# Kernel tuning notes

Hardware: AMD Instinct MI355X
Metric: run time of the kernel (lower is better)

Reference implementation:

```python
import jax, jax.numpy as jnp
import numpy as np

N = 100000  # nodes
E = 1600000  # edges


def gcn_conv(x, W, b, src, dst, n_nodes):
    """PyG-style GCNConv: add self-loops, symmetric norm, linear, scatter-add, bias."""
    h = x @ W  # [N, F_out]
    loop = jnp.arange(n_nodes, dtype=src.dtype)
    s = jnp.concatenate([src, loop])  # source nodes (messages flow src -> dst)
    d = jnp.concatenate([dst, loop])
    deg = jax.ops.segment_sum(jnp.ones_like(d, dtype=h.dtype), d, num_segments=n_nodes)
    dinv = jnp.where(deg > 0, jax.lax.rsqrt(deg), 0.0)
    norm = dinv[s] * dinv[d]  # [E+N]
    msgs = h[s] * norm[:, None]  # [E+N, F_out] -- dominant memory traffic
    out = jax.ops.segment_sum(msgs, d, num_segments=n_nodes)
    return out + b


def setup_inputs() -> dict:
    key = jax.random.key(0)
    k1, k2, k3, k4 = jax.random.split(key, 4)
    x = jax.random.normal(k1, (N, 128), dtype=jnp.float32)
    edge_index = jax.random.randint(k2, (2, E), 0, N, dtype=jnp.int32)
    W1 = jax.random.normal(k3, (128, 64), dtype=jnp.float32) * (1.0 / np.sqrt(128))
    b1 = jnp.zeros((64,), dtype=jnp.float32)
    W2 = jax.random.normal(k4, (64, 16), dtype=jnp.float32) * (1.0 / np.sqrt(64))
    b2 = jnp.zeros((16,), dtype=jnp.float32)
    return {"x": x, "edge_index": edge_index, "W1": W1, "b1": b1, "W2": W2, "b2": b2}


def reference(x, edge_index, W1, b1, W2, b2):
    src, dst = edge_index[0], edge_index[1]
    h = gcn_conv(x, W1, b1, src, dst, N)
    h = jax.nn.leaky_relu(h, negative_slope=0.2)
    # dropout is identity in eval mode
    h = gcn_conv(h, W2, b2, src, dst, N)
    return jax.nn.log_softmax(h, axis=-1)
```

## Files before the change

### kernel.cpp

```cpp
#include <hip/hip_runtime.h>
#include <math.h>


#define CHUNK 4096
#define BSHIFT 9
#define BMASK 511
#define CAP 9216

typedef __bf16 bf16x8 __attribute__((ext_vector_type(8)));
typedef float f32x4 __attribute__((ext_vector_type(4)));

__device__ __forceinline__ unsigned f2b(float f) {
  unsigned u = __float_as_uint(f);
  return (u + 0x7FFF + ((u >> 16) & 1)) >> 16;
}

__global__ void binit_kernel(int* __restrict__ gbcursor, int nbc,
                             unsigned* __restrict__ h1s, int n) {
  int b = blockIdx.x * 256 + threadIdx.x;
  if (b < nbc) gbcursor[b] = b * CAP;
  if (blockIdx.x == 0 && threadIdx.x < 32) h1s[(size_t)n * 32 + threadIdx.x] = 0u;
}

__global__ __launch_bounds__(256) void scatterA_kernel(const int* __restrict__ src,
                                                       const int* __restrict__ dst,
                                                       int E, int nbc,
                                                       int* __restrict__ gbcursor,
                                                       int* __restrict__ tmp) {
  __shared__ int hist[256];
  __shared__ int segcur[256];
  int tid = threadIdx.x;
  int estart = blockIdx.x * CHUNK;
  int eend = min(E, estart + CHUNK);
  hist[tid] = 0;
  __syncthreads();
  for (int i = estart + tid; i < eend; i += 256)
    atomicAdd(&hist[dst[i] >> BSHIFT], 1);
  __syncthreads();
  if (tid < nbc) {
    int c = hist[tid];
    segcur[tid] = c ? atomicAdd(&gbcursor[tid], c) : 0;
  }
  __syncthreads();
  for (int i = estart + tid; i < eend; i += 256) {
    int d = dst[i];
    int b = d >> BSHIFT;
    int pos = atomicAdd(&segcur[b], 1);
    if (pos < (b + 1) * CAP)
      tmp[pos] = (src[i] << BSHIFT) | (d & BMASK);
  }
}

__global__ __launch_bounds__(1024) void csrbuild_kernel(const int* __restrict__ tmp,
                                                        const int* __restrict__ gbcursor,
                                                        int n, int* __restrict__ row_start,
                                                        int* __restrict__ degs,
                                                        float* __restrict__ dinv,
                                                        int* __restrict__ csr) {
  __shared__ int nh[512];
  __shared__ int sc[512];
  __shared__ int lcur[512];
  int b = blockIdx.x, tid = threadIdx.x;
  int base = b * CAP;
  int count = min(gbcursor[b] - base, CAP);
  if (tid < 512) nh[tid] = 0;
  __syncthreads();
  for (int i = tid; i < count; i += 1024) atomicAdd(&nh[tmp[base + i] & BMASK], 1);
  __syncthreads();
  int d = 0;
  if (tid < 512) { d = nh[tid]; sc[tid] = d; }
  __syncthreads();
  for (int off = 1; off < 512; off <<= 1) {
    int a = 0;
    if (tid < 512) { a = sc[tid]; if (tid >= off) a += sc[tid - off]; }
    __syncthreads();
    if (tid < 512) sc[tid] = a;
    __syncthreads();
  }
  if (tid < 512) {
    int e0 = base + sc[tid] - d;
    lcur[tid] = e0;
    int v = (b << BSHIFT) + tid;
    if (v < n) {
      row_start[v] = e0; degs[v] = d;
      dinv[v] = rsqrtf((float)(d + 1));
    }
  }
  __syncthreads();
  for (int i = tid; i < count; i += 1024) {
    int val = tmp[base + i];
    int pos = atomicAdd(&lcur[val & BMASK], 1);
    csr[pos] = val >> BSHIFT;
  }
}

__global__ __launch_bounds__(256, 4) void gemm1_kernel(const float* __restrict__ x,
                                                       const float* __restrict__ W1,
                                                       const float* __restrict__ dinv,
                                                       unsigned* __restrict__ h1s, int n) {
  __shared__ unsigned lds_u[64 * 68 * 2];
  unsigned* xs = lds_u;
  unsigned* wt = lds_u + 64 * 68;
  int tid = threadIdx.x;
  int vb = blockIdx.x * 64;
  int nrows = min(64, n - vb);

  const float4* xg = (const float4*)(x + (size_t)vb * 128);
#pragma unroll
  for (int it = 0; it < 8; ++it) {
    int idx = it * 256 + tid;
    int r = idx >> 5, c2 = idx & 31;
    float4 vv = make_float4(0.f, 0.f, 0.f, 0.f);
    if (r < nrows) vv = xg[idx];
    xs[r * 68 + c2 * 2] = (f2b(vv.y) << 16) | f2b(vv.x);
    xs[r * 68 + c2 * 2 + 1] = (f2b(vv.w) << 16) | f2b(vv.z);
  }
  unsigned short* wt16 = (unsigned short*)wt;
  const float4* wg = (const float4*)W1;
#pragma unroll
  for (int it = 0; it < 8; ++it) {
    int idx = it * 256 + tid;
    int k = idx >> 4, n0 = (idx & 15) * 4;
    float4 wv = wg[idx];
    wt16[(n0 + 0) * 136 + k] = (unsigned short)f2b(wv.x);
    wt16[(n0 + 1) * 136 + k] = (unsigned short)f2b(wv.y);
    wt16[(n0 + 2) * 136 + k] = (unsigned short)f2b(wv.z);
    wt16[(n0 + 3) * 136 + k] = (unsigned short)f2b(wv.w);
  }
  __syncthreads();

  int lane = tid & 63, wid = tid >> 6;
  int m16 = lane & 15, quad = lane >> 4;
  const unsigned* xp = xs + (wid * 16 + m16) * 68 + quad * 4;
  const unsigned* wp = wt + m16 * 68 + quad * 4;
  f32x4 acc[4] = {};
#pragma unroll
  for (int ks = 0; ks < 4; ++ks) {
    bf16x8 a = *(const bf16x8*)(xp + ks * 16);
#pragma unroll
    for (int nt = 0; nt < 4; ++nt) {
      bf16x8 b = *(const bf16x8*)(wp + nt * 16 * 68 + ks * 16);
      acc[nt] = __builtin_amdgcn_mfma_f32_16x16x32_bf16(a, b, acc[nt], 0, 0, 0);
    }
  }
  int rbase = vb + wid * 16 + quad * 4;
  float dvv[4];
#pragma unroll
  for (int reg = 0; reg < 4; ++reg) {
    int row = rbase + reg;
    dvv[reg] = (row < n) ? dinv[row] : 0.f;
  }
  unsigned short* h16 = (unsigned short*)h1s;
#pragma unroll
  for (int nt = 0; nt < 4; ++nt) {
    int col = nt * 16 + m16;
#pragma unroll
    for (int reg = 0; reg < 4; ++reg) {
      int row = rbase + reg;
      if (row < n)
        h16[(size_t)row * 64 + col] = (unsigned short)f2b(dvv[reg] * acc[nt][reg]);
    }
  }
}

struct f2 { float x, y; };
__device__ __forceinline__ void addu(f2& a, unsigned u) {
  a.x += __uint_as_float(u << 16);
  a.y += __uint_as_float(u);
}
__device__ __forceinline__ void addu4(f2* a, uint4 g) {
  addu(a[0], g.x); addu(a[1], g.y); addu(a[2], g.z); addu(a[3], g.w);
}

__global__ __launch_bounds__(256) void agg1_kernel(const uint4* __restrict__ h1s4,
                                                   const float* __restrict__ dinv,
                                                   const int* __restrict__ row_start,
                                                   const int* __restrict__ degs,
                                                   const int* __restrict__ csr,
                                                   const float* __restrict__ b1,
                                                   const float* __restrict__ W2,
                                                   unsigned* __restrict__ t, int n) {
  __shared__ float W2s[64 * 17];
  __shared__ float b1s[64];
  __shared__ float a_s[4][2][64];
  for (int i = threadIdx.x; i < 1024; i += 256)
    W2s[(i >> 4) * 17 + (i & 15)] = W2[i];
  if (threadIdx.x < 64) b1s[threadIdx.x] = b1[threadIdx.x];
  if (blockIdx.x == 0 && threadIdx.x < 8) t[(size_t)n * 8 + threadIdx.x] = 0u;
  __syncthreads();

  int wave = threadIdx.x >> 6, lane = threadIdx.x & 63;
  int half = lane >> 5, sub = lane & 31;
  int e = sub >> 3, c = sub & 7;
  int j = sub & 15, grp = (sub >> 4) & 1;

  for (int vbase = blockIdx.x * 8; vbase < n; vbase += gridDim.x * 8) {
    int v = vbase + wave * 2 + half;
    bool valid = (v < n);
    int vc = valid ? v : 0;
    int i = row_start[vc];
    int e1 = i + (valid ? degs[vc] : 0);
    float dv = valid ? dinv[vc] : 0.f;

    f2 a0[4];
#pragma unroll
    for (int k = 0; k < 4; ++k) a0[k] = {0.f, 0.f};
    {
      int s = (valid && sub < 8) ? v : n;
      addu4(a0, h1s4[(size_t)s * 8 + c]);
    }
    while (__any(i < e1)) {
      int i0 = i + e, i1 = i + 4 + e;
      int s0v = csr[i0];
      int s1v = csr[i1];
      int s0 = (i0 < e1) ? s0v : n;
      int s1 = (i1 < e1) ? s1v : n;
      uint4 g0 = h1s4[(size_t)s0 * 8 + c];
      uint4 g1 = h1s4[(size_t)s1 * 8 + c];
      addu4(a0, g0);
      addu4(a0, g1);
      i += 8;
    }
#pragma unroll
    for (int m = 8; m <= 16; m <<= 1) {
#pragma unroll
      for (int k = 0; k < 4; ++k) {
        a0[k].x += __shfl_xor(a0[k].x, m, 64);
        a0[k].y += __shfl_xor(a0[k].y, m, 64);
      }
    }
    if (sub < 8) {
#pragma unroll
      for (int k = 0; k < 4; ++k) {
        float z0 = fmaf(dv, a0[k].x, b1s[8 * sub + 2 * k]);
        float z1 = fmaf(dv, a0[k].y, b1s[8 * sub + 2 * k + 1]);
        a_s[wave][half][8 * sub + 2 * k] = fmaxf(z0, 0.2f * z0);
        a_s[wave][half][8 * sub + 2 * k + 1] = fmaxf(z1, 0.2f * z1);
      }
    }
    float p = 0.f;
#pragma unroll
    for (int q = 0; q < 16; ++q) {
      int f = grp * 16 + q;
      p = fmaf(a_s[wave][half][f], W2s[f * 17 + j], p);
    }
#pragma unroll
    for (int q = 0; q < 16; ++q) {
      int f = 32 + grp * 16 + q;
      p = fmaf(a_s[wave][half][f], W2s[f * 17 + j], p);
    }
    p += __shfl_xor(p, 16, 64);
    float pv = dv * p;
    float po = __shfl_xor(pv, 1, 64);
    if (valid && sub < 16 && !(sub & 1))
      t[(size_t)v * 8 + (sub >> 1)] = (f2b(po) << 16) | f2b(pv);
  }
}

__global__ __launch_bounds__(256) void agg2_kernel(const uint4* __restrict__ t4,
                                                   const float* __restrict__ dinv,
                                                   const int* __restrict__ row_start,
                                                   const int* __restrict__ degs,
                                                   const int* __restrict__ csr,
                                                   const float* __restrict__ b2,
                                                   float* __restrict__ out, int n) {
  int idx = blockIdx.x * 256 + threadIdx.x;
  int v = idx >> 4;
  if (v >= n) return;
  int sub = threadIdx.x & 15;
  int e = sub >> 1, c = sub & 1;
  float dv = dinv[v];
  int e0 = row_start[v], e1 = e0 + degs[v];
  f2 A0[4], A1[4];
#pragma unroll
  for (int k = 0; k < 4; ++k) { A0[k] = {0.f, 0.f}; A1[k] = {0.f, 0.f}; }
  {
    int s = (e == 0) ? v : n;
    addu4(A0, t4[(size_t)s * 2 + c]);
  }
  int i = e0;
  while (i + 8 < e1) {
    int i1 = i + 8 + e;
    int s0 = csr[i + e];
    int s1v = csr[i1];
    int s1 = (i1 < e1) ? s1v : n;
    uint4 g0 = t4[(size_t)s0 * 2 + c];
    uint4 g1 = t4[(size_t)s1 * 2 + c];
    addu4(A0, g0);
    addu4(A1, g1);
    i += 16;
  }
  if (i < e1) {
    int i0 = i + e;
    int sv = csr[i0];
    int s = (i0 < e1) ? sv : n;
    addu4(A0, t4[(size_t)s * 2 + c]);
  }
#pragma unroll
  for (int k = 0; k < 4; ++k) { A0[k].x += A1[k].x; A0[k].y += A1[k].y; }
#pragma unroll
  for (int m = 2; m <= 8; m <<= 1) {
#pragma unroll
    for (int k = 0; k < 4; ++k) {
      A0[k].x += __shfl_xor(A0[k].x, m, 64);
      A0[k].y += __shfl_xor(A0[k].y, m, 64);
    }
  }
  float4 bb0 = ((const float4*)b2)[c * 2];
  float4 bb1 = ((const float4*)b2)[c * 2 + 1];
  float z[8];
  z[0] = fmaf(dv, A0[0].x, bb0.x); z[1] = fmaf(dv, A0[0].y, bb0.y);
  z[2] = fmaf(dv, A0[1].x, bb0.z); z[3] = fmaf(dv, A0[1].y, bb0.w);
  z[4] = fmaf(dv, A0[2].x, bb1.x); z[5] = fmaf(dv, A0[2].y, bb1.y);
  z[6] = fmaf(dv, A0[3].x, bb1.z); z[7] = fmaf(dv, A0[3].y, bb1.w);
  float mx = z[0];
#pragma unroll
  for (int q = 1; q < 8; ++q) mx = fmaxf(mx, z[q]);
  mx = fmaxf(mx, __shfl_xor(mx, 1, 64));
  float ss = 0.f;
#pragma unroll
  for (int q = 0; q < 8; ++q) ss += expf(z[q] - mx);
  ss += __shfl_xor(ss, 1, 64);
  float lg = mx + logf(ss);
  if (e == 0) {
    float4 r0 = make_float4(z[0] - lg, z[1] - lg, z[2] - lg, z[3] - lg);
    float4 r1 = make_float4(z[4] - lg, z[5] - lg, z[6] - lg, z[7] - lg);
    float4* o = (float4*)out + (size_t)v * 4 + c * 2;
    o[0] = r0;
    o[1] = r1;
  }
}

extern "C" void kernel_launch(void* const* d_in, const int* in_sizes, int n_in,
                              void* d_out, int out_size, void* d_ws, size_t ws_size,
                              hipStream_t stream) {
  const float* x = (const float*)d_in[0];
  const int* edge_index = (const int*)d_in[1];
  const float* W1 = (const float*)d_in[2];
  const float* b1 = (const float*)d_in[3];
  const float* W2 = (const float*)d_in[4];
  const float* b2 = (const float*)d_in[5];
  float* out = (float*)d_out;

  int N_ = in_sizes[0] / 128;
  int E_ = in_sizes[1] / 2;
  const int* src = edge_index;
  const int* dst = edge_index + E_;
  int NBc = (N_ + BMASK) >> BSHIFT;

  char* ws = (char*)d_ws;
  size_t off = 0;
  auto take = [&](size_t bytes) {
    void* p = ws + off;
    off += (bytes + 255) & ~(size_t)255;
    return p;
  };
  unsigned* h1s = (unsigned*)take(((size_t)N_ + 1) * 32 * 4);
  size_t t_bytes = ((size_t)N_ + 1) * 8 * 4, tmp_bytes = (size_t)NBc * CAP * 4;
  void* t_union = take(t_bytes > tmp_bytes ? t_bytes : tmp_bytes);
  unsigned* t = (unsigned*)t_union;
  int* tmp = (int*)t_union;
  float* dinv = (float*)take((size_t)N_ * 4);
  int* degs = (int*)take((size_t)N_ * 4);
  int* row_start = (int*)take(((size_t)N_ + 1) * 4);
  int* csr = (int*)take(((size_t)NBc * CAP + 16) * 4);
  int* gbcursor = (int*)take((size_t)NBc * 4);
  (void)ws_size;

  binit_kernel<<<(NBc + 255) / 256, 256, 0, stream>>>(gbcursor, NBc, h1s, N_);
  scatterA_kernel<<<(E_ + CHUNK - 1) / CHUNK, 256, 0, stream>>>(src, dst, E_, NBc,
                                                                gbcursor, tmp);
  csrbuild_kernel<<<NBc, 1024, 0, stream>>>(tmp, gbcursor, N_, row_start, degs,
                                            dinv, csr);
  gemm1_kernel<<<(N_ + 63) / 64, 256, 0, stream>>>(x, W1, dinv, h1s, N_);
  agg1_kernel<<<2048, 256, 0, stream>>>((const uint4*)h1s, dinv, row_start, degs,
                                        csr, b1, W2, t, N_);
  agg2_kernel<<<(N_ * 16 + 255) / 256, 256, 0, stream>>>((const uint4*)t, dinv,
                                                         row_start, degs, csr,
                                                         b2, out, N_);
}
```

Measured before the change: 212.2 us.

## Fuse CSR build into layer-1 aggregation using LDS-resident bucket adjacency

Splits the CSR build into a lightweight degree-count kernel, which feeds dinv to the GEMM, and moves the bucket sort into the layer-1 aggregation kernel. Each 1024-thread block now sorts its 512-node bucket into shared memory and aggregates directly from that local CSR, writing the global CSR only for layer 2. It also prefetches the first 32 neighbor indices and gathers into registers to raise memory-level parallelism in both aggregation kernels. The costs are one extra pass over tmp and a grid of only about 196 large blocks with heavy LDS use, which may reduce occupancy. tmp and t no longer share a buffer.

```diff
diff --git a/kernel.cpp b/kernel.cpp
--- a/kernel.cpp
+++ b/kernel.cpp
@@ -6,6 +6,7 @@
 #define BSHIFT 9
 #define BMASK 511
 #define CAP 9216
+#define CAPP (CAP + 40)
 
 typedef __bf16 bf16x8 __attribute__((ext_vector_type(8)));
 typedef float f32x4 __attribute__((ext_vector_type(4)));
@@ -15,11 +16,24 @@
   return (u + 0x7FFF + ((u >> 16) & 1)) >> 16;
 }
 
+struct f2 { float x, y; };
+__device__ __forceinline__ void addu(f2& a, unsigned u) {
+  a.x += __uint_as_float(u << 16);
+  a.y += __uint_as_float(u & 0xffff0000u);
+}
+__device__ __forceinline__ void addu4(f2* a, uint4 g) {
+  addu(a[0], g.x); addu(a[1], g.y); addu(a[2], g.z); addu(a[3], g.w);
+}
+
 __global__ void binit_kernel(int* __restrict__ gbcursor, int nbc,
-                             unsigned* __restrict__ h1s, int n) {
+                             unsigned* __restrict__ h1s, unsigned* __restrict__ t,
+                             int n) {
   int b = blockIdx.x * 256 + threadIdx.x;
   if (b < nbc) gbcursor[b] = b * CAP;
-  if (blockIdx.x == 0 && threadIdx.x < 32) h1s[(size_t)n * 32 + threadIdx.x] = 0u;
+  if (blockIdx.x == 0) {
+    if (threadIdx.x < 32) h1s[(size_t)n * 32 + threadIdx.x] = 0u;
+    else if (threadIdx.x < 40) t[(size_t)n * 8 + (threadIdx.x - 32)] = 0u;
+  }
 }
 
 __global__ __launch_bounds__(256) void scatterA_kernel(const int* __restrict__ src,
@@ -51,47 +65,19 @@
   }
 }
 
-__global__ __launch_bounds__(1024) void csrbuild_kernel(const int* __restrict__ tmp,
-                                                        const int* __restrict__ gbcursor,
-                                                        int n, int* __restrict__ row_start,
-                                                        int* __restrict__ degs,
-                                                        float* __restrict__ dinv,
-                                                        int* __restrict__ csr) {
+__global__ __launch_bounds__(512) void degcnt_kernel(const int* __restrict__ tmp,
+                                                     const int* __restrict__ gbcursor,
+                                                     float* __restrict__ dinv, int n) {
   __shared__ int nh[512];
-  __shared__ int sc[512];
-  __shared__ int lcur[512];
   int b = blockIdx.x, tid = threadIdx.x;
+  nh[tid] = 0;
+  __syncthreads();
   int base = b * CAP;
   int count = min(gbcursor[b] - base, CAP);
-  if (tid < 512) nh[tid] = 0;
-  __syncthreads();
-  for (int i = tid; i < count; i += 1024) atomicAdd(&nh[tmp[base + i] & BMASK], 1);
-  __syncthreads();
-  int d = 0;
-  if (tid < 512) { d = nh[tid]; sc[tid] = d; }
-  __syncthreads();
-  for (int off = 1; off < 512; off <<= 1) {
-    int a = 0;
-    if (tid < 512) { a = sc[tid]; if (tid >= off) a += sc[tid - off]; }
-    __syncthreads();
-    if (tid < 512) sc[tid] = a;
-    __syncthreads();
-  }
-  if (tid < 512) {
-    int e0 = base + sc[tid] - d;
-    lcur[tid] = e0;
-    int v = (b << BSHIFT) + tid;
-    if (v < n) {
-      row_start[v] = e0; degs[v] = d;
-      dinv[v] = rsqrtf((float)(d + 1));
-    }
-  }
-  __syncthreads();
-  for (int i = tid; i < count; i += 1024) {
-    int val = tmp[base + i];
-    int pos = atomicAdd(&lcur[val & BMASK], 1);
-    csr[pos] = val >> BSHIFT;
-  }
+  for (int i = tid; i < count; i += 512) atomicAdd(&nh[tmp[base + i] & BMASK], 1);
+  __syncthreads();
+  int v = (b << BSHIFT) + tid;
+  if (v < n) dinv[v] = rsqrtf((float)(nh[tid] + 1));
 }
 
 __global__ __launch_bounds__(256, 4) void gemm1_kernel(const float* __restrict__ x,
@@ -163,44 +149,69 @@
   }
 }
 
-struct f2 { float x, y; };
-__device__ __forceinline__ void addu(f2& a, unsigned u) {
-  a.x += __uint_as_float(u << 16);
-  a.y += __uint_as_float(u);
-}
-__device__ __forceinline__ void addu4(f2* a, uint4 g) {
-  addu(a[0], g.x); addu(a[1], g.y); addu(a[2], g.z); addu(a[3], g.w);
-}
-
-__global__ __launch_bounds__(256) void agg1_kernel(const uint4* __restrict__ h1s4,
-                                                   const float* __restrict__ dinv,
-                                                   const int* __restrict__ row_start,
-                                                   const int* __restrict__ degs,
-                                                   const int* __restrict__ csr,
-                                                   const float* __restrict__ b1,
-                                                   const float* __restrict__ W2,
-                                                   unsigned* __restrict__ t, int n) {
+__global__ __launch_bounds__(1024) void agg1_fused_kernel(
+    const int* __restrict__ tmp, const int* __restrict__ gbcursor,
+    const uint4* __restrict__ h1s4, const float* __restrict__ dinv,
+    const float* __restrict__ b1, const float* __restrict__ W2,
+    int* __restrict__ row_start, int* __restrict__ degs, int* __restrict__ csr,
+    unsigned* __restrict__ t, int n) {
+  __shared__ int lcsr[CAPP];
+  __shared__ int nh[512];
+  __shared__ int rs_s[512];
+  __shared__ int lcur[512];
   __shared__ float W2s[64 * 17];
   __shared__ float b1s[64];
-  __shared__ float a_s[4][2][64];
-  for (int i = threadIdx.x; i < 1024; i += 256)
-    W2s[(i >> 4) * 17 + (i & 15)] = W2[i];
-  if (threadIdx.x < 64) b1s[threadIdx.x] = b1[threadIdx.x];
-  if (blockIdx.x == 0 && threadIdx.x < 8) t[(size_t)n * 8 + threadIdx.x] = 0u;
-  __syncthreads();
-
-  int wave = threadIdx.x >> 6, lane = threadIdx.x & 63;
+  __shared__ float a_s[16][2][64];
+  int b = blockIdx.x, tid = threadIdx.x;
+  int base = b * CAP;
+  int count = min(gbcursor[b] - base, CAP);
+
+  if (tid < 512) nh[tid] = 0;
+  W2s[(tid >> 4) * 17 + (tid & 15)] = W2[tid];
+  if (tid < 64) b1s[tid] = b1[tid];
+  __syncthreads();
+  for (int i = tid; i < count; i += 1024) atomicAdd(&nh[tmp[base + i] & BMASK], 1);
+  __syncthreads();
+  int d = 0;
+  if (tid < 512) { d = nh[tid]; rs_s[tid] = d; }
+  __syncthreads();
+  for (int off = 1; off < 512; off <<= 1) {
+    int a = 0;
+    if (tid < 512) { a = rs_s[tid]; if (tid >= off) a += rs_s[tid - off]; }
+    __syncthreads();
+    if (tid < 512) rs_s[tid] = a;
+    __syncthreads();
+  }
+  if (tid < 512) {
+    int e0 = rs_s[tid] - d;
+    lcur[tid] = e0;
+    rs_s[tid] = e0;
+    int v = (b << BSHIFT) + tid;
+    if (v < n) { row_start[v] = base + e0; degs[v] = d; }
+  }
+  __syncthreads();
+  for (int i = tid; i < count; i += 1024) {
+    int val = tmp[base + i];
+    int pos = atomicAdd(&lcur[val & BMASK], 1);
+    lcsr[pos] = val >> BSHIFT;
+  }
+  __syncthreads();
+  for (int i = tid; i < count; i += 1024) csr[base + i] = lcsr[i];
+
+  int wave = tid >> 6, lane = tid & 63;
   int half = lane >> 5, sub = lane & 31;
   int e = sub >> 3, c = sub & 7;
   int j = sub & 15, grp = (sub >> 4) & 1;
 
-  for (int vbase = blockIdx.x * 8; vbase < n; vbase += gridDim.x * 8) {
-    int v = vbase + wave * 2 + half;
+#pragma unroll 1
+  for (int it = 0; it < 16; ++it) {
+    int nl = wave * 32 + it * 2 + half;
+    int v = (b << BSHIFT) + nl;
     bool valid = (v < n);
-    int vc = valid ? v : 0;
-    int i = row_start[vc];
-    int e1 = i + (valid ? degs[vc] : 0);
-    float dv = valid ? dinv[vc] : 0.f;
+    int rs = rs_s[nl];
+    int deg = nh[nl];
+    int e1 = rs + deg;
+    float dv = valid ? dinv[valid ? v : 0] : 0.f;
 
     f2 a0[4];
 #pragma unroll
@@ -209,16 +220,32 @@
       int s = (valid && sub < 8) ? v : n;
       addu4(a0, h1s4[(size_t)s * 8 + c]);
     }
+    int cv0[4], cv1[4];
+#pragma unroll
+    for (int q = 0; q < 4; ++q) {
+      cv0[q] = lcsr[rs + q * 8 + e];
+      cv1[q] = lcsr[rs + q * 8 + 4 + e];
+    }
+    uint4 g[8];
+#pragma unroll
+    for (int q = 0; q < 4; ++q) {
+      int k0 = rs + q * 8 + e, k1 = k0 + 4;
+      int s0 = (k0 < e1) ? cv0[q] : n;
+      int s1 = (k1 < e1) ? cv1[q] : n;
+      g[2 * q] = h1s4[(size_t)s0 * 8 + c];
+      g[2 * q + 1] = h1s4[(size_t)s1 * 8 + c];
+    }
+#pragma unroll
+    for (int k = 0; k < 8; ++k) addu4(a0, g[k]);
+    int i = rs + 32;
     while (__any(i < e1)) {
       int i0 = i + e, i1 = i + 4 + e;
-      int s0v = csr[i0];
-      int s1v = csr[i1];
+      int s0v = lcsr[i0];
+      int s1v = lcsr[i1];
       int s0 = (i0 < e1) ? s0v : n;
       int s1 = (i1 < e1) ? s1v : n;
-      uint4 g0 = h1s4[(size_t)s0 * 8 + c];
-      uint4 g1 = h1s4[(size_t)s1 * 8 + c];
-      addu4(a0, g0);
-      addu4(a0, g1);
+      addu4(a0, h1s4[(size_t)s0 * 8 + c]);
+      addu4(a0, h1s4[(size_t)s1 * 8 + c]);
       i += 8;
     }
 #pragma unroll
@@ -270,34 +297,34 @@
   int sub = threadIdx.x & 15;
   int e = sub >> 1, c = sub & 1;
   float dv = dinv[v];
-  int e0 = row_start[v], e1 = e0 + degs[v];
-  f2 A0[4], A1[4];
-#pragma unroll
-  for (int k = 0; k < 4; ++k) { A0[k] = {0.f, 0.f}; A1[k] = {0.f, 0.f}; }
+  int rs = row_start[v], e1 = rs + degs[v];
+  f2 A0[4];
+#pragma unroll
+  for (int k = 0; k < 4; ++k) A0[k] = {0.f, 0.f};
   {
     int s = (e == 0) ? v : n;
     addu4(A0, t4[(size_t)s * 2 + c]);
   }
-  int i = e0;
-  while (i + 8 < e1) {
-    int i1 = i + 8 + e;
-    int s0 = csr[i + e];
-    int s1v = csr[i1];
-    int s1 = (i1 < e1) ? s1v : n;
-    uint4 g0 = t4[(size_t)s0 * 2 + c];
-    uint4 g1 = t4[(size_t)s1 * 2 + c];
-    addu4(A0, g0);
-    addu4(A1, g1);
-    i += 16;
-  }
-  if (i < e1) {
+  int cv[4];
+#pragma unroll
+  for (int q = 0; q < 4; ++q) cv[q] = csr[rs + q * 8 + e];
+  uint4 g[4];
+#pragma unroll
+  for (int q = 0; q < 4; ++q) {
+    int k = rs + q * 8 + e;
+    int s = (k < e1) ? cv[q] : n;
+    g[q] = t4[(size_t)s * 2 + c];
+  }
+#pragma unroll
+  for (int k = 0; k < 4; ++k) addu4(A0, g[k]);
+  int i = rs + 32;
+  while (i < e1) {
     int i0 = i + e;
     int sv = csr[i0];
     int s = (i0 < e1) ? sv : n;
     addu4(A0, t4[(size_t)s * 2 + c]);
-  }
-#pragma unroll
-  for (int k = 0; k < 4; ++k) { A0[k].x += A1[k].x; A0[k].y += A1[k].y; }
+    i += 8;
+  }
 #pragma unroll
   for (int m = 2; m <= 8; m <<= 1) {
 #pragma unroll
@@ -356,25 +383,23 @@
     return p;
   };
   unsigned* h1s = (unsigned*)take(((size_t)N_ + 1) * 32 * 4);
-  size_t t_bytes = ((size_t)N_ + 1) * 8 * 4, tmp_bytes = (size_t)NBc * CAP * 4;
-  void* t_union = take(t_bytes > tmp_bytes ? t_bytes : tmp_bytes);
-  unsigned* t = (unsigned*)t_union;
-  int* tmp = (int*)t_union;
+  unsigned* t = (unsigned*)take(((size_t)N_ + 1) * 8 * 4);
+  int* tmp = (int*)take((size_t)NBc * CAP * 4);
+  int* csr = (int*)take(((size_t)NBc * CAP + 64) * 4);
   float* dinv = (float*)take((size_t)N_ * 4);
   int* degs = (int*)take((size_t)N_ * 4);
-  int* row_start = (int*)take(((size_t)N_ + 1) * 4);
-  int* csr = (int*)take(((size_t)NBc * CAP + 16) * 4);
+  int* row_start = (int*)take((size_t)N_ * 4);
   int* gbcursor = (int*)take((size_t)NBc * 4);
   (void)ws_size;
 
-  binit_kernel<<<(NBc + 255) / 256, 256, 0, stream>>>(gbcursor, NBc, h1s, N_);
+  binit_kernel<<<(NBc + 255) / 256, 256, 0, stream>>>(gbcursor, NBc, h1s, t, N_);
   scatterA_kernel<<<(E_ + CHUNK - 1) / CHUNK, 256, 0, stream>>>(src, dst, E_, NBc,
                                                                 gbcursor, tmp);
-  csrbuild_kernel<<<NBc, 1024, 0, stream>>>(tmp, gbcursor, N_, row_start, degs,
-                                            dinv, csr);
+  degcnt_kernel<<<NBc, 512, 0, stream>>>(tmp, gbcursor, dinv, N_);
   gemm1_kernel<<<(N_ + 63) / 64, 256, 0, stream>>>(x, W1, dinv, h1s, N_);
-  agg1_kernel<<<2048, 256, 0, stream>>>((const uint4*)h1s, dinv, row_start, degs,
-                                        csr, b1, W2, t, N_);
+  agg1_fused_kernel<<<NBc, 1024, 0, stream>>>(tmp, gbcursor, (const uint4*)h1s,
+                                              dinv, b1, W2, row_start, degs, csr,
+                                              t, N_);
   agg2_kernel<<<(N_ * 16 + 255) / 256, 256, 0, stream>>>((const uint4*)t, dinv,
                                                          row_start, degs, csr,
                                                          b2, out, N_);
```

Result: faster. 200.4 us (-5.6%).
